# Kernel tuning notes

Measured on AMD Instinct MI355X. Metric: run time of the kernel, lower is better.

Reference implementation:

```python
import jax, jax.numpy as jnp
import numpy as np

EMBED_DIM = 256
NUM_HEADS = 8
NB = 8          # number of scenes (batches)
LQ = 256        # queries per scene
LS = 4096       # source points per scene
LN_EPS = 1e-5


def setup_inputs() -> dict:
    key = jax.random.key(0)
    ks = jax.random.split(key, 8)
    d = EMBED_DIM
    n_q, n_s = NB * LQ, NB * LS
    w_scale = d ** -0.5  # xavier-ish
    return {
        "source": jax.random.normal(ks[0], (n_s, d), jnp.float32),
        "query": jax.random.normal(ks[1], (n_q, d), jnp.float32),
        "source_pe": 0.1 * jax.random.normal(ks[2], (n_s, d), jnp.float32),
        "query_pe": 0.1 * jax.random.normal(ks[3], (n_q, d), jnp.float32),
        "in_proj_w": w_scale * jax.random.normal(ks[4], (3 * d, d), jnp.float32),
        "in_proj_b": jnp.zeros((3 * d,), jnp.float32),
        "out_w": w_scale * jax.random.normal(ks[5], (d, d), jnp.float32),
        "out_b": jnp.zeros((d,), jnp.float32),
        "ln_w": jnp.ones((d,), jnp.float32),
        "ln_b": jnp.zeros((d,), jnp.float32),
        # sorted equal-size segments: token i belongs to scene i // L
        "source_batch": (jnp.arange(n_s, dtype=jnp.int32) // LS).astype(jnp.int32),
        "query_batch": (jnp.arange(n_q, dtype=jnp.int32) // LQ).astype(jnp.int32),
        "B": NB,
    }


def reference(source, query, source_pe, query_pe, in_proj_w, in_proj_b,
              out_w, out_b, ln_w, ln_b, source_batch, query_batch, B):
    d = source.shape[-1]
    H = NUM_HEADS
    hd = d // H
    Lq = query.shape[0] // B
    Ls = source.shape[0] // B

    # batch ids are sorted equal segments -> per-scene gather == reshape
    q_in = (query + query_pe).reshape(B, Lq, d)   # q with pos embed
    k_in = (source + source_pe).reshape(B, Ls, d) # k with pos embed
    v_in = source.reshape(B, Ls, d)               # v without pos embed

    Wq, Wk, Wv = jnp.split(in_proj_w, 3, axis=0)
    bq, bk, bv = jnp.split(in_proj_b, 3)

    q = (q_in @ Wq.T + bq).reshape(B, Lq, H, hd)
    k = (k_in @ Wk.T + bk).reshape(B, Ls, H, hd)
    v = (v_in @ Wv.T + bv).reshape(B, Ls, H, hd)

    scores = jnp.einsum('bqhd,bkhd->bhqk', q, k) * (hd ** -0.5)
    attn = jax.nn.softmax(scores, axis=-1)
    o = jnp.einsum('bhqk,bkhd->bqhd', attn, v).reshape(B, Lq, d)
    o = o @ out_w.T + out_b

    # residual (dropout is identity at p=0) + LayerNorm
    res = o + query.reshape(B, Lq, d)
    mu = jnp.mean(res, axis=-1, keepdims=True)
    var = jnp.var(res, axis=-1, keepdims=True)
    y = (res - mu) * jax.lax.rsqrt(var + LN_EPS) * ln_w + ln_b
    return y.reshape(-1, d)
```

## Files before the change

kernel.cpp:

```cpp
#include <hip/hip_runtime.h>
#include <hip/hip_bf16.h>

typedef __bf16 bf16;
typedef __bf16 bf16x4 __attribute__((ext_vector_type(4)));
typedef __bf16 bf16x8 __attribute__((ext_vector_type(8)));
typedef float f32x4 __attribute__((ext_vector_type(4)));

#define D 256
#define NHEAD 8
#define HD 32
#define NB_ 8
#define LQ_ 256
#define LS_ 4096
#define MQ (NB_ * LQ_)
#define MS (NB_ * LS_)

#define QSCALE 0.25500527f

__global__ __launch_bounds__(256) void prep(
    const float* __restrict__ source, const float* __restrict__ source_pe,
    const float* __restrict__ query, const float* __restrict__ query_pe,
    const float* __restrict__ w_in, const float* __restrict__ w_out,
    bf16* __restrict__ SPb, bf16* __restrict__ Sb, bf16* __restrict__ QPb,
    bf16* __restrict__ Wb)
{
    const int NS4 = MS * D / 4;
    const int NQ4 = MQ * D / 4;
    const int NW4 = (768 * 256 + 256 * 256) / 4;
    const int total = NS4 + NQ4 + NW4;
    for (int i = blockIdx.x * 256 + threadIdx.x; i < total; i += gridDim.x * 256) {
        if (i < NS4) {
            const float4 s = ((const float4*)source)[i];
            const float4 p = ((const float4*)source_pe)[i];
            bf16x4 osp;
            osp[0] = (bf16)(s.x + p.x); osp[1] = (bf16)(s.y + p.y);
            osp[2] = (bf16)(s.z + p.z); osp[3] = (bf16)(s.w + p.w);
            ((bf16x4*)SPb)[i] = osp;
            bf16x4 os;
            os[0] = (bf16)s.x; os[1] = (bf16)s.y;
            os[2] = (bf16)s.z; os[3] = (bf16)s.w;
            ((bf16x4*)Sb)[i] = os;
        } else if (i < NS4 + NQ4) {
            const int j = i - NS4;
            const float4 s = ((const float4*)query)[j];
            const float4 p = ((const float4*)query_pe)[j];
            bf16x4 o;
            o[0] = (bf16)(s.x + p.x); o[1] = (bf16)(s.y + p.y);
            o[2] = (bf16)(s.z + p.z); o[3] = (bf16)(s.w + p.w);
            ((bf16x4*)QPb)[j] = o;
        } else {
            const int j = i - NS4 - NQ4;
            const float4 v = (j < 49152) ? ((const float4*)w_in)[j]
                                         : ((const float4*)w_out)[j - 49152];
            bf16x4 o;
            o[0] = (bf16)v.x; o[1] = (bf16)v.y; o[2] = (bf16)v.z; o[3] = (bf16)v.w;
            ((bf16x4*)Wb)[j] = o;
        }
    }
}

__global__ __launch_bounds__(256, 4) void gemm_proj(
    const bf16* __restrict__ SPb, const bf16* __restrict__ Sb,
    const bf16* __restrict__ QPb, const bf16* __restrict__ Wb,
    const float* __restrict__ in_proj_b,
    bf16* __restrict__ Kt, bf16* __restrict__ Vt2, bf16* __restrict__ Qb,
    int mode)
{
    __shared__ bf16 As[128][72];
    __shared__ bf16 Bs[128][72];
    const int tid = threadIdx.x, lane = tid & 63, wid = tid >> 6;
    const int wm = wid >> 1, wn = wid & 1;
    const int g = lane >> 4, q15 = lane & 15;
    const int id = blockIdx.x;

    const bf16* A; const bf16* W; const float* bias; bf16* out;
    int omode, mblk, nblk;
    if (mode == 0) {
        if (id < 512) {
            A = SPb; W = Wb + 256 * D; bias = in_proj_b + 256; out = Kt;
            mblk = id >> 1; nblk = id & 1; omode = 1;
        } else {
            A = QPb; W = Wb; bias = in_proj_b; out = Qb;
            mblk = (id - 512) >> 1; nblk = id & 1; omode = 0;
        }
    } else {
        A = Sb; W = Wb + 512 * D; bias = in_proj_b + 512; out = Vt2;
        mblk = id >> 1; nblk = id & 1; omode = 2;
    }

    f32x4 acc[4][4];
    #pragma unroll
    for (int i = 0; i < 4; ++i)
        #pragma unroll
        for (int j = 0; j < 4; ++j) acc[i][j] = (f32x4){0.f, 0.f, 0.f, 0.f};

    const size_t arow0 = (size_t)mblk * 128;
    const int brow0 = nblk * 128;

    for (int kk = 0; kk < 4; ++kk) {
        const int d0 = kk * 64;
        #pragma unroll
        for (int i = 0; i < 4; ++i) {
            const int idx = i * 256 + tid;
            const int r = idx >> 3, c = (idx & 7) * 8;
            *(bf16x8*)&As[r][c] = *(const bf16x8*)&A[(arow0 + r) * D + d0 + c];
            *(bf16x8*)&Bs[r][c] = *(const bf16x8*)&W[(size_t)(brow0 + r) * D + d0 + c];
        }
        __syncthreads();
        #pragma unroll
        for (int h2 = 0; h2 < 2; ++h2) {
            const int ko = h2 * 32 + g * 8;
            bf16x8 af[4], bfr[4];
            #pragma unroll
            for (int i = 0; i < 4; ++i)
                af[i] = *(const bf16x8*)&As[wm * 64 + i * 16 + q15][ko];
            #pragma unroll
            for (int j = 0; j < 4; ++j)
                bfr[j] = *(const bf16x8*)&Bs[wn * 64 + j * 16 + q15][ko];
            #pragma unroll
            for (int i = 0; i < 4; ++i)
                #pragma unroll
                for (int j = 0; j < 4; ++j)
                    acc[i][j] = __builtin_amdgcn_mfma_f32_16x16x32_bf16(
                        af[i], bfr[j], acc[i][j], 0, 0, 0);
        }
        __syncthreads();
    }

    if (omode == 0) {
        #pragma unroll
        for (int i = 0; i < 4; ++i)
            #pragma unroll
            for (int j = 0; j < 4; ++j) {
                const int n_g = nblk * 128 + wn * 64 + j * 16 + q15;
                const float b = bias[n_g];
                #pragma unroll
                for (int r = 0; r < 4; ++r) {
                    const size_t m_g = arow0 + wm * 64 + i * 16 + g * 4 + r;
                    out[m_g * D + n_g] = (bf16)((acc[i][j][r] + b) * QSCALE);
                }
            }
    } else if (omode == 1) {
        #pragma unroll
        for (int i = 0; i < 4; ++i)
            #pragma unroll
            for (int j = 0; j < 4; ++j) {
                const int n_g = nblk * 128 + wn * 64 + j * 16 + q15;
                const int h = n_g >> 5, d = n_g & 31;
                const int gp = d >> 3, e = d & 7;
                const float b = bias[n_g];
                #pragma unroll
                for (int r = 0; r < 4; ++r) {
                    const size_t m_g = arow0 + wm * 64 + i * 16 + g * 4 + r;
                    const int bb = (int)(m_g >> 12);
                    const int c = (int)((m_g & 4095) >> 6);
                    const int kl = (int)(m_g & 63);
                    const int t = ((kl >> 5) << 1) | ((kl >> 2) & 1);
                    const int q15p = ((kl >> 3) & 3) * 4 + (kl & 3);
                    out[((size_t)(bb * 8 + h) * 64 + c) * 2048
                        + t * 512 + (gp * 16 + q15p) * 8 + e] = (bf16)(acc[i][j][r] + b);
                }
            }
    } else {
        #pragma unroll
        for (int i = 0; i < 4; ++i)
            #pragma unroll
            for (int j = 0; j < 4; ++j) {
                const int n_g = nblk * 128 + wn * 64 + j * 16 + q15;
                const int h = n_g >> 5, d = n_g & 31;
                const int dt = d >> 4, q15p = d & 15;
                const float b = bias[n_g];
                const size_t m_g0 = arow0 + wm * 64 + i * 16 + g * 4;
                const int bb = (int)(m_g0 >> 12);
                const int c = (int)((m_g0 & 4095) >> 6);
                const int kl0 = (int)(m_g0 & 63);
                const int half = kl0 >> 5, gp = (kl0 >> 3) & 3, e0 = kl0 & 7;
                const int f = dt * 2 + half;
                bf16x4 o;
                #pragma unroll
                for (int r = 0; r < 4; ++r) o[r] = (bf16)(acc[i][j][r] + b);
                *(bf16x4*)&out[((size_t)(bb * 8 + h) * 64 + c) * 2048
                               + f * 512 + (gp * 16 + q15p) * 8 + e0] = o;
            }
    }
}

template<int S>
__global__ __launch_bounds__(256, 4) void attn_kernel(
    const bf16* __restrict__ Qb, const bf16* __restrict__ Kt,
    const bf16* __restrict__ Vt2,
    float* __restrict__ accp, float* __restrict__ lp)
{
    const int tid = threadIdx.x, lane = tid & 63, wid = tid >> 6;
    const int q15 = lane & 15, g = lane >> 4;
    const int bid = blockIdx.x;
    const int h = bid & 7;
    const int inner = bid >> 3;
    const int split = inner % S;
    const int tmp = inner / S;
    const int qt = tmp & 1;
    const int b = tmp >> 1;
    constexpr int CHUNKS = LS_ / S / 64;

    const int q0 = b * LQ_ + qt * 128 + wid * 32;
    const bf16x8 qfA = *(const bf16x8*)&Qb[(size_t)(q0 + q15) * D + h * HD + g * 8];
    const bf16x8 qfB = *(const bf16x8*)&Qb[(size_t)(q0 + 16 + q15) * D + h * HD + g * 8];

    const f32x4 minit = (f32x4){-8.f, -8.f, -8.f, -8.f};
    const size_t cbase = ((size_t)(b * 8 + h) * 64 + split * CHUNKS) * 2048;
    const bf16* kp = Kt + cbase + lane * 8;
    const bf16* vp = Vt2 + cbase + lane * 8;

    float lA = 0.f, lB = 0.f;
    f32x4 accA0 = (f32x4){0.f, 0.f, 0.f, 0.f};
    f32x4 accA1 = (f32x4){0.f, 0.f, 0.f, 0.f};
    f32x4 accB0 = (f32x4){0.f, 0.f, 0.f, 0.f};
    f32x4 accB1 = (f32x4){0.f, 0.f, 0.f, 0.f};

    for (int kc = 0; kc < CHUNKS; ++kc) {
        const size_t co = (size_t)kc * 2048;

        bf16x8 kf[4], vf[4];
        #pragma unroll
        for (int t = 0; t < 4; ++t) kf[t] = *(const bf16x8*)&kp[co + t * 512];
        #pragma unroll
        for (int f = 0; f < 4; ++f) vf[f] = *(const bf16x8*)&vp[co + f * 512];

        f32x4 sA[4], sB[4];
        #pragma unroll
        for (int t = 0; t < 4; ++t)
            sA[t] = __builtin_amdgcn_mfma_f32_16x16x32_bf16(kf[t], qfA, minit, 0, 0, 0);
        #pragma unroll
        for (int t = 0; t < 4; ++t)
            sB[t] = __builtin_amdgcn_mfma_f32_16x16x32_bf16(kf[t], qfB, minit, 0, 0, 0);

        bf16x8 paA0, paA1, paB0, paB1;
        #pragma unroll
        for (int r = 0; r < 4; ++r) {
            const float a0 = exp2f(sA[0][r]);
            const float a1 = exp2f(sA[1][r]);
            const float a2 = exp2f(sA[2][r]);
            const float a3 = exp2f(sA[3][r]);
            lA += (a0 + a1) + (a2 + a3);
            paA0[r] = (bf16)a0; paA0[4 + r] = (bf16)a1;
            paA1[r] = (bf16)a2; paA1[4 + r] = (bf16)a3;
            const float b0 = exp2f(sB[0][r]);
            const float b1 = exp2f(sB[1][r]);
            const float b2 = exp2f(sB[2][r]);
            const float b3 = exp2f(sB[3][r]);
            lB += (b0 + b1) + (b2 + b3);
            paB0[r] = (bf16)b0; paB0[4 + r] = (bf16)b1;
            paB1[r] = (bf16)b2; paB1[4 + r] = (bf16)b3;
        }

        accA0 = __builtin_amdgcn_mfma_f32_16x16x32_bf16(paA0, vf[0], accA0, 0, 0, 0);
        accA0 = __builtin_amdgcn_mfma_f32_16x16x32_bf16(paA1, vf[1], accA0, 0, 0, 0);
        accA1 = __builtin_amdgcn_mfma_f32_16x16x32_bf16(paA0, vf[2], accA1, 0, 0, 0);
        accA1 = __builtin_amdgcn_mfma_f32_16x16x32_bf16(paA1, vf[3], accA1, 0, 0, 0);
        accB0 = __builtin_amdgcn_mfma_f32_16x16x32_bf16(paB0, vf[0], accB0, 0, 0, 0);
        accB0 = __builtin_amdgcn_mfma_f32_16x16x32_bf16(paB1, vf[1], accB0, 0, 0, 0);
        accB1 = __builtin_amdgcn_mfma_f32_16x16x32_bf16(paB0, vf[2], accB1, 0, 0, 0);
        accB1 = __builtin_amdgcn_mfma_f32_16x16x32_bf16(paB1, vf[3], accB1, 0, 0, 0);
    }

    lA += __shfl_xor(lA, 16);
    lA += __shfl_xor(lA, 32);
    lB += __shfl_xor(lB, 16);
    lB += __shfl_xor(lB, 32);

    const int qg16 = qt * 8 + wid * 2;
    const int taskA = (b * 8 + h) * 16 + qg16;
    const size_t baseA = ((size_t)(taskA * S + split) * 64 + lane) * 8;
    *(f32x4*)&accp[baseA]     = accA0;
    *(f32x4*)&accp[baseA + 4] = accA1;
    const size_t baseB = ((size_t)((taskA + 1) * S + split) * 64 + lane) * 8;
    *(f32x4*)&accp[baseB]     = accB0;
    *(f32x4*)&accp[baseB + 4] = accB1;
    if (lane < 16) {
        lp[(taskA * S + split) * 16 + lane] = lA;
        lp[((taskA + 1) * S + split) * 16 + lane] = lB;
    }
}

template<int S>
__global__ __launch_bounds__(256) void attn_combine(
    const float* __restrict__ accp, const float* __restrict__ lp,
    bf16* __restrict__ Ob)
{
    const int tid = threadIdx.x, lane = tid & 63, wid = tid >> 6;
    const int task = blockIdx.x * 4 + wid;
    const int g = lane >> 4, q15 = lane & 15;

    f32x4 o0 = (f32x4){0.f, 0.f, 0.f, 0.f};
    f32x4 o1 = (f32x4){0.f, 0.f, 0.f, 0.f};
    float ll = 0.f;
    #pragma unroll
    for (int s = 0; s < S; ++s) {
        const size_t base = ((size_t)(task * S + s) * 64 + lane) * 8;
        o0 += *(const f32x4*)&accp[base];
        o1 += *(const f32x4*)&accp[base + 4];
        if (lane < 16) ll += lp[(task * S + s) * 16 + lane];
    }

    const int b = task >> 7, h = (task >> 4) & 7, qg = task & 15;
    #pragma unroll
    for (int r = 0; r < 4; ++r) {
        const float inv = 1.f / __shfl(ll, g * 4 + r);
        const size_t row = (size_t)b * LQ_ + qg * 16 + g * 4 + r;
        Ob[row * D + h * HD + q15]      = (bf16)(o0[r] * inv);
        Ob[row * D + h * HD + 16 + q15] = (bf16)(o1[r] * inv);
    }
}

__global__ __launch_bounds__(256) void out_ln_kernel(
    const bf16* __restrict__ Ob, const bf16* __restrict__ Wout,
    const float* __restrict__ out_b, const float* __restrict__ query,
    const float* __restrict__ lnw, const float* __restrict__ lnb,
    float* __restrict__ out)
{
    __shared__ bf16 As[128][72];
    __shared__ bf16 Bs[256][72];
    __shared__ float red[2][128][2];
    const int tid = threadIdx.x, lane = tid & 63, wid = tid >> 6;
    const int wm = wid >> 1, wn = wid & 1;
    const int g = lane >> 4, q15 = lane & 15;
    const int mblk = blockIdx.x;

    f32x4 acc[4][8];
    #pragma unroll
    for (int i = 0; i < 4; ++i)
        #pragma unroll
        for (int j = 0; j < 8; ++j) acc[i][j] = (f32x4){0.f, 0.f, 0.f, 0.f};

    for (int kk = 0; kk < 4; ++kk) {
        const int d0 = kk * 64;
        #pragma unroll
        for (int i = 0; i < 4; ++i) {
            const int idx = i * 256 + tid;
            const int r = idx >> 3, c = (idx & 7) * 8;
            *(bf16x8*)&As[r][c] =
                *(const bf16x8*)&Ob[(size_t)(mblk * 128 + r) * D + d0 + c];
        }
        #pragma unroll
        for (int i = 0; i < 8; ++i) {
            const int idx = i * 256 + tid;
            const int r = idx >> 3, c = (idx & 7) * 8;
            *(bf16x8*)&Bs[r][c] = *(const bf16x8*)&Wout[(size_t)r * D + d0 + c];
        }
        __syncthreads();
        #pragma unroll
        for (int h2 = 0; h2 < 2; ++h2) {
            const int ko = h2 * 32 + g * 8;
            bf16x8 af[4], bfr[8];
            #pragma unroll
            for (int i = 0; i < 4; ++i)
                af[i] = *(const bf16x8*)&As[wm * 64 + i * 16 + q15][ko];
            #pragma unroll
            for (int j = 0; j < 8; ++j)
                bfr[j] = *(const bf16x8*)&Bs[wn * 128 + j * 16 + q15][ko];
            #pragma unroll
            for (int i = 0; i < 4; ++i)
                #pragma unroll
                for (int j = 0; j < 8; ++j)
                    acc[i][j] = __builtin_amdgcn_mfma_f32_16x16x32_bf16(
                        af[i], bfr[j], acc[i][j], 0, 0, 0);
        }
        __syncthreads();
    }

    float bl[8], lw[8], lbv[8];
    #pragma unroll
    for (int j = 0; j < 8; ++j) {
        const int n = wn * 128 + j * 16 + q15;
        bl[j] = out_b[n]; lw[j] = lnw[n]; lbv[j] = lnb[n];
    }

    #pragma unroll
    for (int i = 0; i < 4; ++i) {
        #pragma unroll
        for (int r = 0; r < 4; ++r) {
            const size_t m = (size_t)mblk * 128 + wm * 64 + i * 16 + g * 4 + r;
            float s = 0.f, sq = 0.f;
            #pragma unroll
            for (int j = 0; j < 8; ++j) {
                const float v = acc[i][j][r] + bl[j] + query[m * D + wn * 128 + j * 16 + q15];
                acc[i][j][r] = v;
                s += v; sq += v * v;
            }
            s += __shfl_xor(s, 1);  sq += __shfl_xor(sq, 1);
            s += __shfl_xor(s, 2);  sq += __shfl_xor(sq, 2);
            s += __shfl_xor(s, 4);  sq += __shfl_xor(sq, 4);
            s += __shfl_xor(s, 8);  sq += __shfl_xor(sq, 8);
            if (q15 == i * 4 + r) {
                red[wn][wm * 64 + i * 16 + g * 4 + r][0] = s;
                red[wn][wm * 64 + i * 16 + g * 4 + r][1] = sq;
            }
        }
    }
    __syncthreads();

    #pragma unroll
    for (int i = 0; i < 4; ++i)
        #pragma unroll
        for (int r = 0; r < 4; ++r) {
            const int row = wm * 64 + i * 16 + g * 4 + r;
            const float s  = red[0][row][0] + red[1][row][0];
            const float sq = red[0][row][1] + red[1][row][1];
            const float mean = s * (1.f / 256.f);
            const float var  = sq * (1.f / 256.f) - mean * mean;
            const float inv  = rsqrtf(var + 1e-5f);
            const size_t m = (size_t)mblk * 128 + row;
            #pragma unroll
            for (int j = 0; j < 8; ++j)
                out[m * D + wn * 128 + j * 16 + q15] =
                    (acc[i][j][r] - mean) * inv * lw[j] + lbv[j];
        }
}

extern "C" void kernel_launch(void* const* d_in, const int* in_sizes, int n_in,
                              void* d_out, int out_size, void* d_ws, size_t ws_size,
                              hipStream_t stream) {
    (void)in_sizes; (void)n_in; (void)out_size; (void)ws_size;
    const float* source    = (const float*)d_in[0];
    const float* query     = (const float*)d_in[1];
    const float* source_pe = (const float*)d_in[2];
    const float* query_pe  = (const float*)d_in[3];
    const float* in_proj_w = (const float*)d_in[4];
    const float* in_proj_b = (const float*)d_in[5];
    const float* out_w     = (const float*)d_in[6];
    const float* out_b     = (const float*)d_in[7];
    const float* ln_w      = (const float*)d_in[8];
    const float* ln_b      = (const float*)d_in[9];

    constexpr int S = 8;
    bf16* Wb  = (bf16*)d_ws;
    bf16* QPb = Wb + 1024 * 256;
    bf16* Qb  = QPb + (size_t)MQ * D;
    bf16* Kt  = Qb + (size_t)MQ * D;
    bf16* SPb = Kt + (size_t)MS * D;
    bf16* Sb  = SPb + (size_t)MS * D;
    bf16* Vt2   = SPb;
    float* accp = (float*)Sb;
    float* lp   = (float*)QPb;
    bf16* Ob    = Kt;
    float* outp = (float*)d_out;

    prep<<<dim3(2048), dim3(256), 0, stream>>>(
        source, source_pe, query, query_pe, in_proj_w, out_w,
        SPb, Sb, QPb, Wb);
    gemm_proj<<<dim3(544), dim3(256), 0, stream>>>(
        SPb, Sb, QPb, Wb, in_proj_b, Kt, Vt2, Qb, 0);
    gemm_proj<<<dim3(512), dim3(256), 0, stream>>>(
        SPb, Sb, QPb, Wb, in_proj_b, Kt, Vt2, Qb, 1);
    attn_kernel<S><<<dim3(1024), dim3(256), 0, stream>>>(Qb, Kt, Vt2, accp, lp);
    attn_combine<S><<<dim3(256), dim3(256), 0, stream>>>(accp, lp, Ob);
    out_ln_kernel<<<dim3(16), dim3(256), 0, stream>>>(
        Ob, Wb + 768 * 256, out_b, query, ln_w, ln_b, outp);
}
```

Baseline: 96.44 us.

## Merge projection launches, stage K stores through LDS, store attention partials in bf16

The K/V/Q projection GEMMs now run as a single 1056-block launch. Before, V's output aliased the SPb buffer that the K projection read, which forced two launches; the workspace is re-laid out with separate buffers so that aliasing is gone. The K epilogue now scatters into shared memory first and then writes contiguous 16-byte vectors to global memory, replacing scattered 2-byte stores. Split-attention partial accumulators are stored in bf16 instead of fp32, halving that traffic at the cost of some precision in the combine step.

Result: faster. 87.52 us (-9.2%).

```diff
diff --git a/kernel.cpp b/kernel.cpp
--- a/kernel.cpp
+++ b/kernel.cpp
@@ -63,11 +63,11 @@
     const bf16* __restrict__ SPb, const bf16* __restrict__ Sb,
     const bf16* __restrict__ QPb, const bf16* __restrict__ Wb,
     const float* __restrict__ in_proj_b,
-    bf16* __restrict__ Kt, bf16* __restrict__ Vt2, bf16* __restrict__ Qb,
-    int mode)
+    bf16* __restrict__ Kt, bf16* __restrict__ Vt2, bf16* __restrict__ Qb)
 {
-    __shared__ bf16 As[128][72];
-    __shared__ bf16 Bs[128][72];
+    __shared__ __align__(16) bf16 smem[2][128][72];
+    bf16 (*As)[72] = smem[0];
+    bf16 (*Bs)[72] = smem[1];
     const int tid = threadIdx.x, lane = tid & 63, wid = tid >> 6;
     const int wm = wid >> 1, wn = wid & 1;
     const int g = lane >> 4, q15 = lane & 15;
@@ -75,17 +75,15 @@
 
     const bf16* A; const bf16* W; const float* bias; bf16* out;
     int omode, mblk, nblk;
-    if (mode == 0) {
-        if (id < 512) {
-            A = SPb; W = Wb + 256 * D; bias = in_proj_b + 256; out = Kt;
-            mblk = id >> 1; nblk = id & 1; omode = 1;
-        } else {
-            A = QPb; W = Wb; bias = in_proj_b; out = Qb;
-            mblk = (id - 512) >> 1; nblk = id & 1; omode = 0;
-        }
+    if (id < 512) {
+        A = SPb; W = Wb + 256 * D; bias = in_proj_b + 256; out = Kt;
+        mblk = id >> 1; nblk = id & 1; omode = 1;
+    } else if (id < 1024) {
+        A = Sb; W = Wb + 512 * D; bias = in_proj_b + 512; out = Vt2;
+        mblk = (id - 512) >> 1; nblk = id & 1; omode = 2;
     } else {
-        A = Sb; W = Wb + 512 * D; bias = in_proj_b + 512; out = Vt2;
-        mblk = id >> 1; nblk = id & 1; omode = 2;
+        A = QPb; W = Wb; bias = in_proj_b; out = Qb;
+        mblk = (id - 1024) >> 1; nblk = id & 1; omode = 0;
     }
 
     f32x4 acc[4][4];
@@ -141,26 +139,37 @@
                 }
             }
     } else if (omode == 1) {
+        bf16* Ls = &smem[0][0][0];
         #pragma unroll
         for (int i = 0; i < 4; ++i)
             #pragma unroll
             for (int j = 0; j < 4; ++j) {
-                const int n_g = nblk * 128 + wn * 64 + j * 16 + q15;
-                const int h = n_g >> 5, d = n_g & 31;
+                const int n_loc = wn * 64 + j * 16 + q15;
+                const int h_loc = n_loc >> 5, d = n_loc & 31;
                 const int gp = d >> 3, e = d & 7;
-                const float b = bias[n_g];
+                const float b = bias[nblk * 128 + n_loc];
                 #pragma unroll
                 for (int r = 0; r < 4; ++r) {
-                    const size_t m_g = arow0 + wm * 64 + i * 16 + g * 4 + r;
-                    const int bb = (int)(m_g >> 12);
-                    const int c = (int)((m_g & 4095) >> 6);
-                    const int kl = (int)(m_g & 63);
+                    const int m_loc = wm * 64 + i * 16 + g * 4 + r;
+                    const int c_loc = m_loc >> 6, kl = m_loc & 63;
                     const int t = ((kl >> 5) << 1) | ((kl >> 2) & 1);
                     const int q15p = ((kl >> 3) & 3) * 4 + (kl & 3);
-                    out[((size_t)(bb * 8 + h) * 64 + c) * 2048
-                        + t * 512 + (gp * 16 + q15p) * 8 + e] = (bf16)(acc[i][j][r] + b);
+                    Ls[(h_loc * 2 + c_loc) * 2048 + t * 512
+                       + (gp * 16 + q15p) * 8 + e] = (bf16)(acc[i][j][r] + b);
                 }
             }
+        __syncthreads();
+        const int bb = (int)(arow0 >> 12);
+        const int c0 = (int)((arow0 & 4095) >> 6);
+        const int h0 = (nblk * 128) >> 5;
+        #pragma unroll
+        for (int p = 0; p < 8; ++p) {
+            const int idx = p * 2048 + tid * 8;
+            const int blk = idx >> 11, within = idx & 2047;
+            *(bf16x8*)&out[((size_t)(bb * 8 + h0 + (blk >> 1)) * 64
+                            + c0 + (blk & 1)) * 2048 + within]
+                = *(const bf16x8*)&Ls[idx];
+        }
     } else {
         #pragma unroll
         for (int i = 0; i < 4; ++i)
@@ -189,7 +198,7 @@
 __global__ __launch_bounds__(256, 4) void attn_kernel(
     const bf16* __restrict__ Qb, const bf16* __restrict__ Kt,
     const bf16* __restrict__ Vt2,
-    float* __restrict__ accp, float* __restrict__ lp)
+    bf16* __restrict__ accp, float* __restrict__ lp)
 {
     const int tid = threadIdx.x, lane = tid & 63, wid = tid >> 6;
     const int q15 = lane & 15, g = lane >> 4;
@@ -271,11 +280,17 @@
     const int qg16 = qt * 8 + wid * 2;
     const int taskA = (b * 8 + h) * 16 + qg16;
     const size_t baseA = ((size_t)(taskA * S + split) * 64 + lane) * 8;
-    *(f32x4*)&accp[baseA]     = accA0;
-    *(f32x4*)&accp[baseA + 4] = accA1;
     const size_t baseB = ((size_t)((taskA + 1) * S + split) * 64 + lane) * 8;
-    *(f32x4*)&accp[baseB]     = accB0;
-    *(f32x4*)&accp[baseB + 4] = accB1;
+    bf16x4 oA0, oA1, oB0, oB1;
+    #pragma unroll
+    for (int r = 0; r < 4; ++r) {
+        oA0[r] = (bf16)accA0[r]; oA1[r] = (bf16)accA1[r];
+        oB0[r] = (bf16)accB0[r]; oB1[r] = (bf16)accB1[r];
+    }
+    *(bf16x4*)&accp[baseA]     = oA0;
+    *(bf16x4*)&accp[baseA + 4] = oA1;
+    *(bf16x4*)&accp[baseB]     = oB0;
+    *(bf16x4*)&accp[baseB + 4] = oB1;
     if (lane < 16) {
         lp[(taskA * S + split) * 16 + lane] = lA;
         lp[((taskA + 1) * S + split) * 16 + lane] = lB;
@@ -284,7 +299,7 @@
 
 template<int S>
 __global__ __launch_bounds__(256) void attn_combine(
-    const float* __restrict__ accp, const float* __restrict__ lp,
+    const bf16* __restrict__ accp, const float* __restrict__ lp,
     bf16* __restrict__ Ob)
 {
     const int tid = threadIdx.x, lane = tid & 63, wid = tid >> 6;
@@ -297,8 +312,9 @@
     #pragma unroll
     for (int s = 0; s < S; ++s) {
         const size_t base = ((size_t)(task * S + s) * 64 + lane) * 8;
-        o0 += *(const f32x4*)&accp[base];
-        o1 += *(const f32x4*)&accp[base + 4];
+        const bf16x8 v = *(const bf16x8*)&accp[base];
+        #pragma unroll
+        for (int r = 0; r < 4; ++r) { o0[r] += (float)v[r]; o1[r] += (float)v[4 + r]; }
         if (lane < 16) ll += lp[(task * S + s) * 16 + lane];
     }
 
@@ -433,25 +449,23 @@
     const float* ln_b      = (const float*)d_in[9];
 
     constexpr int S = 8;
-    bf16* Wb  = (bf16*)d_ws;
-    bf16* QPb = Wb + 1024 * 256;
-    bf16* Qb  = QPb + (size_t)MQ * D;
-    bf16* Kt  = Qb + (size_t)MQ * D;
-    bf16* SPb = Kt + (size_t)MS * D;
-    bf16* Sb  = SPb + (size_t)MS * D;
-    bf16* Vt2   = SPb;
-    float* accp = (float*)Sb;
-    float* lp   = (float*)QPb;
-    bf16* Ob    = Kt;
+    bf16* Wb   = (bf16*)d_ws;
+    bf16* QPb  = Wb + 1024 * 256;
+    bf16* Qb   = QPb + (size_t)MQ * D;
+    bf16* Kt   = Qb + (size_t)MQ * D;
+    bf16* Vt2  = Kt + (size_t)MS * D;
+    bf16* SPb  = Vt2 + (size_t)MS * D;
+    bf16* Sb   = SPb + (size_t)MS * D;
+    bf16* Ob   = Sb + (size_t)MS * D;
+    bf16* accp = Ob + (size_t)MQ * D;
+    float* lp  = (float*)(accp + (size_t)1024 * S * 64 * 8);
     float* outp = (float*)d_out;
 
     prep<<<dim3(2048), dim3(256), 0, stream>>>(
         source, source_pe, query, query_pe, in_proj_w, out_w,
         SPb, Sb, QPb, Wb);
-    gemm_proj<<<dim3(544), dim3(256), 0, stream>>>(
-        SPb, Sb, QPb, Wb, in_proj_b, Kt, Vt2, Qb, 0);
-    gemm_proj<<<dim3(512), dim3(256), 0, stream>>>(
-        SPb, Sb, QPb, Wb, in_proj_b, Kt, Vt2, Qb, 1);
+    gemm_proj<<<dim3(1056), dim3(256), 0, stream>>>(
+        SPb, Sb, QPb, Wb, in_proj_b, Kt, Vt2, Qb);
     attn_kernel<S><<<dim3(1024), dim3(256), 0, stream>>>(Qb, Kt, Vt2, accp, lp);
     attn_combine<S><<<dim3(256), dim3(256), 0, stream>>>(accp, lp, Ob);
     out_ln_kernel<<<dim3(16), dim3(256), 0, stream>>>(
```
